# Performance work log

Measured on AMD Instinct MI355X. Metric: run time of the kernel, lower is better.

Reference implementation:

```python
import jax, jax.numpy as jnp
import numpy as np
from jax import lax

B, T, IN = 32, 512, 32
SNN, TS, HID, HOR = 128, 4, 128, 96
K = 3
THR = 1.0
EPS = 1e-5


def _spike(x):
    # heaviside: fires when (mem - threshold) > 0
    return (x > 0).astype(x.dtype)


def _lif_scan(xs, beta, thr):
    """snntorch Leaky (reset_mechanism='subtract'): mem_t = beta*mem_{t-1} + x_t - spk_{t-1}*thr; spk_t = H(mem_t - thr).
    xs: (S, B, C); beta: (C,). Returns spikes (S,B,C) and membrane (S,B,C)."""
    def step(carry, x):
        mem, rst = carry
        mem = beta * mem + x - rst * thr
        spk = _spike(mem - thr)
        return (mem, lax.stop_gradient(spk)), (spk, mem)
    z = jnp.zeros(xs.shape[1:], xs.dtype)
    _, (spks, mems) = lax.scan(step, (z, z), xs)
    return spks, mems


def setup_inputs() -> dict:
    key = jax.random.key(0)
    ks = jax.random.split(key, 10)
    def rn(k, shape, scale=0.05):
        return jax.random.normal(k, shape, dtype=jnp.float32) * scale
    return {
        "x": jax.random.normal(ks[0], (B, T, IN), dtype=jnp.float32),
        "conv_w": rn(ks[1], (SNN * TS, IN, K)),
        "conv_b": jnp.zeros((SNN * TS,), jnp.float32),
        "bn1_g": jnp.ones((SNN * TS,), jnp.float32),
        "bn1_b": jnp.zeros((SNN * TS,), jnp.float32),
        "beta1": jnp.full((SNN,), 0.9, jnp.float32),
        "bn2_g": jnp.ones((SNN,), jnp.float32),
        "bn2_b": jnp.zeros((SNN,), jnp.float32),
        "beta2": jnp.full((SNN,), 0.9, jnp.float32),
        "gru_wih": rn(ks[2], (3 * HID, IN + SNN)),
        "gru_whh": rn(ks[3], (3 * HID, HID)),
        "gru_bih": jnp.zeros((3 * HID,), jnp.float32),
        "gru_bhh": jnp.zeros((3 * HID,), jnp.float32),
        "q_w": rn(ks[4], (HID, HID)), "q_b": jnp.zeros((HID,), jnp.float32),
        "k_w": rn(ks[5], (HID, HID)), "k_b": jnp.zeros((HID,), jnp.float32),
        "v_w": rn(ks[6], (HID, HID)), "v_b": jnp.zeros((HID,), jnp.float32),
        "bn3_g": jnp.ones((HID,), jnp.float32),
        "bn3_b": jnp.zeros((HID,), jnp.float32),
        "head_w": rn(ks[7], (HOR, HID)),
        "head_b": jnp.zeros((HOR,), jnp.float32),
    }


def reference(x, conv_w, conv_b, bn1_g, bn1_b, beta1, bn2_g, bn2_b, beta2,
              gru_wih, gru_whh, gru_bih, gru_bhh, q_w, q_b, k_w, k_b, v_w, v_b,
              bn3_g, bn3_b, head_w, head_b):
    beta1 = jnp.clip(beta1, 0.0, 0.99)
    beta2 = jnp.clip(beta2, 0.0, 0.99)
    # --- ConvSpikeEncoder: Conv1d -> BatchNorm1d (training stats) -> LIF scan ---
    h = lax.conv_general_dilated(x.transpose(0, 2, 1), conv_w, (1,), [(K // 2, K // 2)],
                                 dimension_numbers=('NCH', 'OIH', 'NCH'))
    h = h + conv_b[None, :, None]  # (B, SNN*TS, T)
    m = h.mean((0, 2), keepdims=True)
    v = jnp.var(h, (0, 2), keepdims=True)
    h = (h - m) * lax.rsqrt(v + EPS) * bn1_g[None, :, None] + bn1_b[None, :, None]
    # (B, SNN*TS, T) -> (T*TS, B, SNN), step index = t*TS + s
    h = h.transpose(0, 2, 1).reshape(B, T * TS, SNN).transpose(1, 0, 2)
    spk_enc, _ = _lif_scan(h, beta1, THR)  # (T*TS, B, SNN)
    # --- per-step BatchNorm1d over batch dim, then second LIF ---
    m2 = spk_enc.mean(1, keepdims=True)
    v2 = jnp.var(spk_enc, 1, keepdims=True)
    h2 = (spk_enc - m2) * lax.rsqrt(v2 + EPS) * bn2_g + bn2_b
    _, mem_rec = _lif_scan(h2, beta2, THR)  # (T*TS, B, SNN)
    # --- downsample membrane: mean over TS sub-steps ---
    mem_down = mem_rec.transpose(1, 0, 2).reshape(B, T, TS, SNN).mean(2)  # (B, T, SNN)
    hc = jnp.concatenate([x, mem_down], -1)  # (B, T, IN+SNN)
    # --- GRU (PyTorch gate order r,z,n) ---
    def gstep(hprev, xt):
        gi = xt @ gru_wih.T + gru_bih
        gh = hprev @ gru_whh.T + gru_bhh
        ir, iz, inn = jnp.split(gi, 3, -1)
        hr, hz, hn = jnp.split(gh, 3, -1)
        r = jax.nn.sigmoid(ir + hr)
        zg = jax.nn.sigmoid(iz + hz)
        n = jnp.tanh(inn + r * hn)
        hnew = (1.0 - zg) * n + zg * hprev
        return hnew, hnew
    _, gru_seq = lax.scan(gstep, jnp.zeros((B, HID), x.dtype), hc.transpose(1, 0, 2))
    g = gru_seq.transpose(1, 0, 2)  # (B, T, HID)
    # --- SpikingAttention: sigmoid(QK^T*scale) @ V, mean over T, BatchNorm ---
    Q = g @ q_w.T + q_b
    Kk = g @ k_w.T + k_b
    V = g @ v_w.T + v_b
    attn = jax.nn.sigmoid(jnp.einsum('btc,bsc->bts', Q, Kk) * (HID ** -0.5))
    out = jnp.einsum('bts,bsc->btc', attn, V).mean(1)  # (B, HID)
    m3 = out.mean(0, keepdims=True)
    v3 = jnp.var(out, 0, keepdims=True)
    out = (out - m3) * lax.rsqrt(v3 + EPS) * bn3_g + bn3_b
    return out @ head_w.T + head_b  # (B, HOR)
```

## Files before the change

kernel.cpp:

```cpp
#include <hip/hip_runtime.h>
#include <math.h>

#define EPSV 1e-5f

#if __has_builtin(__builtin_amdgcn_exp2f)
#define EXP2F(x) __builtin_amdgcn_exp2f(x)
#else
#define EXP2F(x) exp2f(x)
#endif
#if __has_builtin(__builtin_amdgcn_rcpf)
#define RCPF(x) __builtin_amdgcn_rcpf(x)
#else
#define RCPF(x) (1.0f/(x))
#endif

__device__ __forceinline__ float fsigmoid(float x){
  return RCPF(1.0f + EXP2F(-1.4426950408889634f * x));
}
__device__ __forceinline__ float ftanh(float x){
  return RCPF(0.5f + 0.5f * EXP2F(-2.8853900817779268f * x)) - 1.0f;
}
__device__ __forceinline__ unsigned short f2bf(float f){
  unsigned u = __float_as_uint(f);
  return (unsigned short)((u + 0x7FFFu + ((u >> 16) & 1u)) >> 16);
}

typedef __attribute__((ext_vector_type(8))) short bf16x8;
typedef __attribute__((ext_vector_type(8))) short s16x8;
typedef __attribute__((ext_vector_type(4))) float f32x4;
typedef __attribute__((ext_vector_type(2))) _Float16 f16x2;
typedef __attribute__((ext_vector_type(8))) _Float16 f16x8;

#if __has_builtin(__builtin_amdgcn_fdot2)
#define FDOT2(a,b,c) __builtin_amdgcn_fdot2(a,b,c,false)
#else
__device__ __forceinline__ float FDOT2(f16x2 a, f16x2 b, float c){
  return c + (float)a[0]*(float)b[0] + (float)a[1]*(float)b[1];
}
#endif

__device__ __forceinline__ float dot8(f16x8 w, f16x8 h, float acc){
  f16x2 w0 = {w[0],w[1]}, w1 = {w[2],w[3]}, w2 = {w[4],w[5]}, w3 = {w[6],w[7]};
  f16x2 h0 = {h[0],h[1]}, h1 = {h[2],h[3]}, h2 = {h[4],h[5]}, h3 = {h[6],h[7]};
  acc = FDOT2(w0,h0,acc); acc = FDOT2(w1,h1,acc);
  acc = FDOT2(w2,h2,acc); acc = FDOT2(w3,h3,acc);
  return acc;
}

__global__ __launch_bounds__(256) void k_conv(const float* __restrict__ x, const float* __restrict__ w,
        const float* __restrict__ cb, float* __restrict__ hp, float* __restrict__ s1g,
        float* __restrict__ s2g, unsigned short* __restrict__ x_bf){
  __shared__ float xs[32*321];
  __shared__ float ws[32*97];
  __shared__ float bs[32];
  const int tid = threadIdx.x;
  const int t0 = blockIdx.x * 8;
  const int n0 = blockIdx.y * 8;
  for (int idx = tid; idx < 32*10*32; idx += 256){
    int bq = idx / 320; int rem = idx - bq*320; int tt = rem >> 5; int i = rem & 31;
    int tg = t0 - 1 + tt;
    float v = 0.f;
    if (tg >= 0 && tg < 512) v = x[(bq*512 + tg)*32 + i];
    xs[bq*321 + tt*32 + i] = v;
  }
  for (int idx = tid; idx < 32*96; idx += 256){
    int row = idx / 96; int within = idx - row*96;
    int ss = row >> 3; int nl = row & 7;
    int c = ss*128 + n0 + nl;
    ws[row*97 + within] = w[c*96 + within];
  }
  if (tid < 32){
    int ss = tid >> 3, nl = tid & 7;
    bs[tid] = cb[ss*128 + n0 + nl];
  }
  __syncthreads();
  if (blockIdx.y == 0){
    for (int idx = tid; idx < 32*8*32; idx += 256){
      int bq = idx >> 8; int rem = idx & 255; int tt = rem >> 5; int i = rem & 31;
      x_bf[(bq*512 + t0 + tt)*32 + i] = f2bf(xs[bq*321 + (tt+1)*32 + i]);
    }
  }
  const int b = tid & 31;
  const int nl = tid >> 5;
  float acc[4][8];
  #pragma unroll
  for (int ss = 0; ss < 4; ++ss){
    float bv = bs[ss*8 + nl];
    #pragma unroll
    for (int t = 0; t < 8; ++t) acc[ss][t] = bv;
  }
  for (int i = 0; i < 32; ++i){
    #pragma unroll
    for (int k = 0; k < 3; ++k){
      float w0 = ws[(0*8+nl)*97 + i*3 + k];
      float w1 = ws[(1*8+nl)*97 + i*3 + k];
      float w2 = ws[(2*8+nl)*97 + i*3 + k];
      float w3 = ws[(3*8+nl)*97 + i*3 + k];
      #pragma unroll
      for (int t = 0; t < 8; ++t){
        float xv = xs[b*321 + (t+k)*32 + i];
        acc[0][t] += xv*w0; acc[1][t] += xv*w1; acc[2][t] += xv*w2; acc[3][t] += xv*w3;
      }
    }
  }
  #pragma unroll
  for (int ss = 0; ss < 4; ++ss){
    int n = n0 + nl;
    float s1 = 0.f, s2 = 0.f;
    #pragma unroll
    for (int t = 0; t < 8; ++t){
      float v = acc[ss][t];
      int s = (t0 + t)*4 + ss;
      hp[s*4096 + n*32 + b] = v;
      s1 += v; s2 += v*v;
    }
    #pragma unroll
    for (int off = 1; off < 32; off <<= 1){
      s1 += __shfl_xor(s1, off);
      s2 += __shfl_xor(s2, off);
    }
    if (b == 0){
      int c = ss*128 + n;
      atomicAdd(&s1g[c], s1);
      atomicAdd(&s2g[c], s2);
    }
  }
}

__global__ __launch_bounds__(256) void k_cvt_all(const float* __restrict__ wih,
        const float* __restrict__ qw, const float* __restrict__ kw, const float* __restrict__ vw,
        const float* __restrict__ whh,
        unsigned short* __restrict__ wih_bf, unsigned short* __restrict__ wqkv_bf,
        _Float16* __restrict__ whh_h,
        const float* __restrict__ s1g, const float* __restrict__ s2g,
        const float* __restrict__ g, const float* __restrict__ bb,
        float* __restrict__ a1, float* __restrict__ b1){
  if (blockIdx.x >= 624){
    int c = (blockIdx.x - 624)*256 + threadIdx.x;
    if (c < 512){
      float m = s1g[c] * (1.f/16384.f);
      float v = s2g[c] * (1.f/16384.f) - m*m;
      float sc = g[c] * rsqrtf(v + EPSV);
      a1[c] = sc;
      b1[c] = bb[c] - m*sc;
    }
    return;
  }
  int i = blockIdx.x*256 + threadIdx.x;
  if (i < 61440){ wih_bf[i] = f2bf(wih[i]); return; }
  int r = i - 61440;
  if (r < 16384){ wqkv_bf[r] = f2bf(qw[r]); return; }
  r -= 16384;
  if (r < 16384){ wqkv_bf[16384 + r] = f2bf(kw[r]); return; }
  r -= 16384;
  if (r < 16384){ wqkv_bf[32768 + r] = f2bf(vw[r]); return; }
  r -= 16384;
  if (r < 49152){ whh_h[r] = (_Float16)whh[r]; }
}

__global__ __launch_bounds__(64) void k_lif(const float* __restrict__ hp,
        const float* __restrict__ a1, const float* __restrict__ b1,
        const float* __restrict__ beta1, const float* __restrict__ g2v, const float* __restrict__ b2v,
        const float* __restrict__ beta2, unsigned short* __restrict__ md_t){
  const int tid = threadIdx.x;
  const int b = tid & 31;
  const int n = blockIdx.x * 2 + (tid >> 5);
  float a1r0 = a1[0*128+n], a1r1 = a1[1*128+n], a1r2 = a1[2*128+n], a1r3 = a1[3*128+n];
  float b1r0 = b1[0*128+n], b1r1 = b1[1*128+n], b1r2 = b1[2*128+n], b1r3 = b1[3*128+n];
  float be1 = fminf(fmaxf(beta1[n], 0.f), 0.99f);
  float be2 = fminf(fmaxf(beta2[n], 0.f), 0.99f);
  float g2 = g2v[n], bb2 = b2v[n];
  float m1 = 0.f, r1 = 0.f, m2 = 0.f, r2 = 0.f;
  const float* base = hp + n*32 + b;
  float c0 = base[0], c1 = base[4096], c2 = base[2*4096], c3 = base[3*4096];
  const float* p1 = base + 16384;
  float d0 = p1[0], d1 = p1[4096], d2 = p1[2*4096], d3 = p1[3*4096];
  const float* p2 = base + 2*16384;
  float e0 = p2[0], e1 = p2[4096], e2 = p2[2*4096], e3 = p2[3*4096];

#define LIF_STEP(CV, A1R, B1R) { \
    float x1 = CV*A1R + B1R; \
    m1 = be1*m1 + x1 - r1; \
    bool sp = (m1 > 1.0f); \
    unsigned long long mk = __ballot(sp); \
    float spk = sp ? 1.f : 0.f; r1 = spk; \
    unsigned hf = (tid & 32) ? (unsigned)(mk >> 32) : (unsigned)mk; \
    float mean = (float)__popc(hf) * 0.03125f; \
    float var = mean - mean*mean; \
    float h2 = (spk - mean) * rsqrtf(var + EPSV) * g2 + bb2; \
    m2 = be2*m2 + h2 - r2; \
    r2 = (m2 > 1.0f) ? 1.f : 0.f; \
    accd += m2; }

  for (int t = 0; t < 512; ++t){
    float f0 = 0.f, f1 = 0.f, f2 = 0.f, f3 = 0.f;
    if (t < 509){
      const float* nb = base + (size_t)(t+3)*16384;
      f0 = nb[0]; f1 = nb[4096]; f2 = nb[2*4096]; f3 = nb[3*4096];
    }
    float accd = 0.f;
    LIF_STEP(c0, a1r0, b1r0)
    LIF_STEP(c1, a1r1, b1r1)
    LIF_STEP(c2, a1r2, b1r2)
    LIF_STEP(c3, a1r3, b1r3)
    md_t[((t*128) + n)*32 + b] = f2bf(accd * 0.25f);
    c0 = d0; c1 = d1; c2 = d2; c3 = d3;
    d0 = e0; d1 = e1; d2 = e2; d3 = e3;
    e0 = f0; e1 = f1; e2 = f2; e3 = f3;
  }
#undef LIF_STEP
}

__global__ __launch_bounds__(256) void k_mm_gi(const unsigned short* __restrict__ xbf,
        const unsigned short* __restrict__ md_t, const unsigned short* __restrict__ wihbf,
        const float* __restrict__ bih, float* __restrict__ gi2){
  const int tid = threadIdx.x;
  const int w = tid >> 6, l = tid & 63;
  const int c16 = l & 15, kg = l >> 4;
  const int m0 = (blockIdx.x*4 + w) * 16;
  const int mrow = m0 + c16;
  const int bb = mrow >> 9, tt = mrow & 511;
  bf16x8 a0 = *(const bf16x8*)&xbf[(size_t)mrow*32 + kg*8];
  const unsigned short* mt = md_t + (size_t)tt*4096 + bb;
  unsigned short tmp[4][8];
  #pragma unroll
  for (int f = 0; f < 4; ++f)
    #pragma unroll
    for (int e = 0; e < 8; ++e)
      tmp[f][e] = mt[(kg*8 + f*32 + e)*32];
  bf16x8 a1 = *(bf16x8*)tmp[0];
  bf16x8 a2 = *(bf16x8*)tmp[1];
  bf16x8 a3 = *(bf16x8*)tmp[2];
  bf16x8 a4 = *(bf16x8*)tmp[3];
  for (int nt2 = 0; nt2 < 8; ++nt2){
    int n0 = nt2*16;
    const unsigned short* wr = &wihbf[(size_t)(      n0 + c16)*160 + kg*8];
    const unsigned short* wz = &wihbf[(size_t)(128 + n0 + c16)*160 + kg*8];
    const unsigned short* wn = &wihbf[(size_t)(256 + n0 + c16)*160 + kg*8];
    f32x4 ar = {0.f,0.f,0.f,0.f}, az = {0.f,0.f,0.f,0.f}, an = {0.f,0.f,0.f,0.f};
    #pragma unroll
    for (int c = 0; c < 5; ++c){
      bf16x8 br = *(const bf16x8*)(wr + c*32);
      bf16x8 bz = *(const bf16x8*)(wz + c*32);
      bf16x8 bn = *(const bf16x8*)(wn + c*32);
      bf16x8 aa = (c == 0) ? a0 : (c == 1) ? a1 : (c == 2) ? a2 : (c == 3) ? a3 : a4;
      ar = __builtin_amdgcn_mfma_f32_16x16x32_bf16(aa, br, ar, 0, 0, 0);
      az = __builtin_amdgcn_mfma_f32_16x16x32_bf16(aa, bz, az, 0, 0, 0);
      an = __builtin_amdgcn_mfma_f32_16x16x32_bf16(aa, bn, an, 0, 0, 0);
    }
    float br_ = bih[n0 + c16], bz_ = bih[128 + n0 + c16], bn_ = bih[256 + n0 + c16];
    int jj = n0 + c16;
    #pragma unroll
    for (int r = 0; r < 4; ++r){
      float4 o = { ar[r] + br_, az[r] + bz_, an[r] + bn_, 0.f };
      *(float4*)&gi2[(size_t)(m0 + kg*4 + r)*512 + jj*4] = o;
    }
  }
}

template<int SEL>
__device__ __forceinline__ float dpp_qp(float x){
  return __int_as_float(__builtin_amdgcn_mov_dpp(__float_as_int(x), SEL, 0xF, 0xF, true));
}
__global__ __launch_bounds__(256, 1) void k_gru(const float* __restrict__ gi2, const _Float16* __restrict__ whh_h,
        const float* __restrict__ bhh, unsigned short* __restrict__ gout_bf){
  const int b = blockIdx.x;
  const int tid = threadIdx.x;
  const int j = tid >> 1;
  const int half = tid & 1;
  const int k0 = half * 64;
  __shared__ _Float16 hs[2][144];
  const _Float16* wbr = whh_h + (size_t)(      j)*128 + k0;
  const _Float16* wbz = whh_h + (size_t)(128 + j)*128 + k0;
  const _Float16* wbn = whh_h + (size_t)(256 + j)*128 + k0;
  f16x8 wr[8], wz[8], wn[8];
  #pragma unroll
  for (int i = 0; i < 8; ++i){
    wr[i] = *(const f16x8*)(wbr + i*8);
    wz[i] = *(const f16x8*)(wbz + i*8);
    wn[i] = *(const f16x8*)(wbn + i*8);
  }
  float bh_r = 0.f, bh_z = 0.f, bh_n = 0.f;
  if (!half){
    bh_r = bhh[j]; bh_z = bhh[128+j]; bh_n = bhh[256+j];
  }
  const float* gib = gi2 + (size_t)b*512*512 + j*4;
  f32x4 G[4], N[4];
  #pragma unroll
  for (int u = 0; u < 4; ++u){
    G[u] = *(const f32x4*)(gib + (size_t)u*512);
    N[u] = *(const f32x4*)(gib + (size_t)(4+u)*512);
  }
  if (tid < 128) hs[0][tid] = (_Float16)0.f;
  float hprev = 0.f;
  __syncthreads();
  for (int g = 0; g < 128; ++g){
    f32x4 N2[4];
    if (g < 126){
      #pragma unroll
      for (int u = 0; u < 4; ++u)
        N2[u] = *(const f32x4*)(gib + (size_t)(4*(g+2)+u)*512);
    } else {
      #pragma unroll
      for (int u = 0; u < 4; ++u) N2[u] = (f32x4){0.f,0.f,0.f,0.f};
    }
    #pragma unroll
    for (int u = 0; u < 4; ++u){
      const int t = g*4 + u;
      const f16x8* hq = (const f16x8*)&hs[t & 1][k0];
      f16x8 h0 = hq[0], h1 = hq[1], h2 = hq[2], h3 = hq[3],
            h4 = hq[4], h5 = hq[5], h6 = hq[6], h7 = hq[7];
      float ar0 = 0.f, ar1 = 0.f, az0 = 0.f, az1 = 0.f, an0 = 0.f, an1 = 0.f;
      ar0 = dot8(wr[0],h0,ar0); ar0 = dot8(wr[1],h1,ar0); ar0 = dot8(wr[2],h2,ar0); ar0 = dot8(wr[3],h3,ar0);
      ar1 = dot8(wr[4],h4,ar1); ar1 = dot8(wr[5],h5,ar1); ar1 = dot8(wr[6],h6,ar1); ar1 = dot8(wr[7],h7,ar1);
      az0 = dot8(wz[0],h0,az0); az0 = dot8(wz[1],h1,az0); az0 = dot8(wz[2],h2,az0); az0 = dot8(wz[3],h3,az0);
      az1 = dot8(wz[4],h4,az1); az1 = dot8(wz[5],h5,az1); az1 = dot8(wz[6],h6,az1); az1 = dot8(wz[7],h7,az1);
      an0 = dot8(wn[0],h0,an0); an0 = dot8(wn[1],h1,an0); an0 = dot8(wn[2],h2,an0); an0 = dot8(wn[3],h3,an0);
      an1 = dot8(wn[4],h4,an1); an1 = dot8(wn[5],h5,an1); an1 = dot8(wn[6],h6,an1); an1 = dot8(wn[7],h7,an1);
      float ar = ar0 + ar1, az = az0 + az1, an = an0 + an1;
      ar += dpp_qp<0xB1>(ar);
      az += dpp_qp<0xB1>(az);
      an += dpp_qp<0xB1>(an);
      if (!half){
        float r = fsigmoid(G[u][0] + ar + bh_r);
        float z = fsigmoid(G[u][1] + az + bh_z);
        float nn = ftanh(G[u][2] + r*(an + bh_n));
        float hn = (1.f - z)*nn + z*hprev;
        hprev = hn;
        hs[(t + 1) & 1][j] = (_Float16)hn;
        gout_bf[((size_t)b*512 + t)*128 + j] = f2bf(hn);
      }
      __syncthreads();
    }
    #pragma unroll
    for (int u = 0; u < 4; ++u){ G[u] = N[u]; N[u] = N2[u]; }
  }
}

__global__ __launch_bounds__(256) void k_mm_qkv(const unsigned short* __restrict__ gbf,
        const unsigned short* __restrict__ wbf, const float* __restrict__ qb2,
        const float* __restrict__ kb2, const float* __restrict__ vb2,
        unsigned short* __restrict__ Qbf, unsigned short* __restrict__ Kbf, float* __restrict__ Vb){
  const int tid = threadIdx.x;
  const int w = tid >> 6, l = tid & 63;
  const int c16 = l & 15, kg = l >> 4;
  const int m0 = (blockIdx.x*4 + w) * 16;
  const unsigned short* gp = &gbf[(size_t)(m0 + c16)*128 + kg*8];
  bf16x8 a0 = *(const bf16x8*)(gp + 0);
  bf16x8 a1 = *(const bf16x8*)(gp + 32);
  bf16x8 a2 = *(const bf16x8*)(gp + 64);
  bf16x8 a3 = *(const bf16x8*)(gp + 96);
  for (int nt = 0; nt < 24; ++nt){
    int n0 = nt*16;
    const unsigned short* wp = &wbf[(size_t)(n0 + c16)*128 + kg*8];
    bf16x8 b0 = *(const bf16x8*)(wp + 0);
    bf16x8 b1 = *(const bf16x8*)(wp + 32);
    bf16x8 b2 = *(const bf16x8*)(wp + 64);
    bf16x8 b3 = *(const bf16x8*)(wp + 96);
    f32x4 acc = {0.f,0.f,0.f,0.f};
    acc = __builtin_amdgcn_mfma_f32_16x16x32_bf16(a0, b0, acc, 0, 0, 0);
    acc = __builtin_amdgcn_mfma_f32_16x16x32_bf16(a1, b1, acc, 0, 0, 0);
    acc = __builtin_amdgcn_mfma_f32_16x16x32_bf16(a2, b2, acc, 0, 0, 0);
    acc = __builtin_amdgcn_mfma_f32_16x16x32_bf16(a3, b3, acc, 0, 0, 0);
    int n = n0 + c16;
    if (n < 128){
      float bias = qb2[n];
      #pragma unroll
      for (int r = 0; r < 4; ++r)
        Qbf[(size_t)(m0 + kg*4 + r)*128 + n] = f2bf(acc[r] + bias);
    } else if (n < 256){
      float bias = kb2[n-128];
      #pragma unroll
      for (int r = 0; r < 4; ++r)
        Kbf[(size_t)(m0 + kg*4 + r)*128 + (n-128)] = f2bf(acc[r] + bias);
    } else {
      float bias = vb2[n-256];
      #pragma unroll
      for (int r = 0; r < 4; ++r)
        Vb[(size_t)(m0 + kg*4 + r)*128 + (n-256)] = acc[r] + bias;
    }
  }
}

__global__ __launch_bounds__(256) void k_attn(const unsigned short* __restrict__ Qbf,
        const unsigned short* __restrict__ Kbf, const float* __restrict__ Vb,
        float* __restrict__ out0){
  __shared__ float avs[64];
  const int tid = threadIdx.x;
  const int b  = blockIdx.x;
  const int st = blockIdx.y;
  const int w  = tid >> 6;
  const int l  = tid & 63;
  const int c16 = l & 15;
  const int kg  = l >> 4;
  const float SC = 0.08838834764831845f;
  const unsigned short* kp = Kbf + ((size_t)(b*512 + st*64 + w*16 + c16))*128 + kg*8;
  bf16x8 a0 = *(const bf16x8*)(kp + 0);
  bf16x8 a1 = *(const bf16x8*)(kp + 32);
  bf16x8 a2 = *(const bf16x8*)(kp + 64);
  bf16x8 a3 = *(const bf16x8*)(kp + 96);
  const unsigned short* qb = Qbf + ((size_t)(b*512 + c16))*128 + kg*8;
  float ps0 = 0.f, ps1 = 0.f, ps2 = 0.f, ps3 = 0.f;
  for (int tt = 0; tt < 32; ++tt){
    const unsigned short* qp = qb + (size_t)tt*16*128;
    bf16x8 b0 = *(const bf16x8*)(qp + 0);
    bf16x8 b1 = *(const bf16x8*)(qp + 32);
    bf16x8 b2 = *(const bf16x8*)(qp + 64);
    bf16x8 b3 = *(const bf16x8*)(qp + 96);
    f32x4 acc = {0.f, 0.f, 0.f, 0.f};
    acc = __builtin_amdgcn_mfma_f32_16x16x32_bf16(a0, b0, acc, 0, 0, 0);
    acc = __builtin_amdgcn_mfma_f32_16x16x32_bf16(a1, b1, acc, 0, 0, 0);
    acc = __builtin_amdgcn_mfma_f32_16x16x32_bf16(a2, b2, acc, 0, 0, 0);
    acc = __builtin_amdgcn_mfma_f32_16x16x32_bf16(a3, b3, acc, 0, 0, 0);
    ps0 += fsigmoid(acc[0]*SC);
    ps1 += fsigmoid(acc[1]*SC);
    ps2 += fsigmoid(acc[2]*SC);
    ps3 += fsigmoid(acc[3]*SC);
  }
  #pragma unroll
  for (int off = 1; off < 16; off <<= 1){
    ps0 += __shfl_xor(ps0, off);
    ps1 += __shfl_xor(ps1, off);
    ps2 += __shfl_xor(ps2, off);
    ps3 += __shfl_xor(ps3, off);
  }
  if (c16 == 0){
    int sl = w*16 + kg*4;
    avs[sl + 0] = ps0 * (1.f/512.f);
    avs[sl + 1] = ps1 * (1.f/512.f);
    avs[sl + 2] = ps2 * (1.f/512.f);
    avs[sl + 3] = ps3 * (1.f/512.f);
  }
  __syncthreads();
  const int c = tid & 127;
  const int sh = tid >> 7;
  const float* vb = Vb + ((size_t)(b*512 + st*64 + sh*32))*128 + c;
  float acc = 0.f;
  #pragma unroll 8
  for (int sl = 0; sl < 32; ++sl)
    acc += avs[sh*32 + sl] * vb[(size_t)sl*128];
  atomicAdd(&out0[b*128 + c], acc);
}

__global__ __launch_bounds__(256) void k_final(const float* __restrict__ out0,
        const float* __restrict__ g3, const float* __restrict__ b3,
        const float* __restrict__ hw, const float* __restrict__ hb, float* __restrict__ out){
  __shared__ float on[2][132];
  const int tid = threadIdx.x;
  const int b0 = blockIdx.x * 2;
  if (tid < 128){
    int c = tid;
    float s = 0.f;
    #pragma unroll 8
    for (int bq = 0; bq < 32; ++bq) s += out0[bq*128 + c];
    float m = s * (1.f/32.f);
    float v = 0.f;
    #pragma unroll 8
    for (int bq = 0; bq < 32; ++bq){ float d = out0[bq*128 + c] - m; v += d*d; }
    v *= (1.f/32.f);
    float sc = g3[c] * rsqrtf(v + EPSV);
    float sh = b3[c] - m*sc;
    on[0][c] = out0[(b0+0)*128 + c]*sc + sh;
    on[1][c] = out0[(b0+1)*128 + c]*sc + sh;
  }
  __syncthreads();
  for (int o = tid; o < 2*96; o += 256){
    int bl = o / 96, hh = o - bl*96;
    float acc = hb[hh];
    for (int k = 0; k < 128; ++k) acc += on[bl][k] * hw[hh*128 + k];
    out[(b0 + bl)*96 + hh] = acc;
  }
}

extern "C" void kernel_launch(void* const* d_in, const int* in_sizes, int n_in,
                              void* d_out, int out_size, void* d_ws, size_t ws_size,
                              hipStream_t stream){
  const float* x      = (const float*)d_in[0];
  const float* conv_w = (const float*)d_in[1];
  const float* conv_b = (const float*)d_in[2];
  const float* bn1_g  = (const float*)d_in[3];
  const float* bn1_b  = (const float*)d_in[4];
  const float* beta1  = (const float*)d_in[5];
  const float* bn2_g  = (const float*)d_in[6];
  const float* bn2_b  = (const float*)d_in[7];
  const float* beta2  = (const float*)d_in[8];
  const float* g_wih  = (const float*)d_in[9];
  const float* g_whh  = (const float*)d_in[10];
  const float* g_bih  = (const float*)d_in[11];
  const float* g_bhh  = (const float*)d_in[12];
  const float* q_w    = (const float*)d_in[13];
  const float* q_b    = (const float*)d_in[14];
  const float* k_w    = (const float*)d_in[15];
  const float* k_b    = (const float*)d_in[16];
  const float* v_w    = (const float*)d_in[17];
  const float* v_b    = (const float*)d_in[18];
  const float* bn3_g  = (const float*)d_in[19];
  const float* bn3_b  = (const float*)d_in[20];
  const float* head_w = (const float*)d_in[21];
  const float* head_b = (const float*)d_in[22];

  char* ws = (char*)d_ws;
  float* hp            = (float*)ws;
  unsigned short* md_t = (unsigned short*)(ws + 37748736);
  unsigned short* g_bf = (unsigned short*)(ws + 37748736);
  unsigned short* x_bf = (unsigned short*)(ws + 41943040);
  unsigned short* wih_bf  = (unsigned short*)(ws + 42991616);
  unsigned short* wqkv_bf = (unsigned short*)(ws + 43114496);
  _Float16* whh_h      = (_Float16*)(ws + 43212800);
  float* s1g  = (float*)(ws + 50331648);
  float* s2g  = (float*)(ws + 50331648 + 2048);
  float* out0 = (float*)(ws + 50331648 + 4096);
  float* a1   = (float*)(ws + 50331648 + 20480);
  float* b1   = (float*)(ws + 50331648 + 22528);
  float* gi2 = (float*)ws;
  unsigned short* Qbf = (unsigned short*)ws;
  unsigned short* Kbf = (unsigned short*)(ws + 4194304);
  float* Vb  = (float*)(ws + 8388608);

  (void)hipMemsetAsync(ws + 50331648, 0, 20480, stream);

  k_conv<<<dim3(64, 16), 256, 0, stream>>>(x, conv_w, conv_b, hp, s1g, s2g, x_bf);
  k_cvt_all<<<626, 256, 0, stream>>>(g_wih, q_w, k_w, v_w, g_whh, wih_bf, wqkv_bf, whh_h,
                                     s1g, s2g, bn1_g, bn1_b, a1, b1);
  k_lif<<<64, 64, 0, stream>>>(hp, a1, b1, beta1, bn2_g, bn2_b, beta2, md_t);
  k_mm_gi<<<256, 256, 0, stream>>>(x_bf, md_t, wih_bf, g_bih, gi2);
  k_gru<<<32, 256, 0, stream>>>(gi2, whh_h, g_bhh, g_bf);
  k_mm_qkv<<<256, 256, 0, stream>>>(g_bf, wqkv_bf, q_b, k_b, v_b, Qbf, Kbf, Vb);
  k_attn<<<dim3(32, 8), 256, 0, stream>>>(Qbf, Kbf, Vb, out0);
  k_final<<<16, 256, 0, stream>>>(out0, bn3_g, bn3_b, head_w, head_b, (float*)d_out);
}
```

Before: 587.4 us.

## Fuse weight conversion into conv, fold BN1 stats into LIF, store GRU gates as bf16

The weight-conversion blocks are appended to the conv launch as extra blocks, which removes one kernel launch. The BN1 scale and shift are now computed inside the LIF kernel straight from the accumulated sums, so the separate a1/b1 buffers are gone. The GRU input-gate precompute is written as bf16 instead of fp32, which halves the traffic into the latency-bound recurrent kernel. The cost is reduced precision in the gate pre-activations, and the conversion blocks now depend on sharing a launch with the conv work.

```diff
diff --git a/kernel.cpp b/kernel.cpp
--- a/kernel.cpp
+++ b/kernel.cpp
@@ -24,9 +24,11 @@
   unsigned u = __float_as_uint(f);
   return (unsigned short)((u + 0x7FFFu + ((u >> 16) & 1u)) >> 16);
 }
+__device__ __forceinline__ float bf2f(unsigned short u){
+  return __uint_as_float(((unsigned)u) << 16);
+}
 
 typedef __attribute__((ext_vector_type(8))) short bf16x8;
-typedef __attribute__((ext_vector_type(8))) short s16x8;
 typedef __attribute__((ext_vector_type(4))) float f32x4;
 typedef __attribute__((ext_vector_type(2))) _Float16 f16x2;
 typedef __attribute__((ext_vector_type(8))) _Float16 f16x8;
@@ -47,15 +49,32 @@
   return acc;
 }
 
-__global__ __launch_bounds__(256) void k_conv(const float* __restrict__ x, const float* __restrict__ w,
+__global__ __launch_bounds__(256) void k_convcvt(const float* __restrict__ x, const float* __restrict__ w,
         const float* __restrict__ cb, float* __restrict__ hp, float* __restrict__ s1g,
-        float* __restrict__ s2g, unsigned short* __restrict__ x_bf){
+        float* __restrict__ s2g, unsigned short* __restrict__ x_bf,
+        const float* __restrict__ wih, const float* __restrict__ qw, const float* __restrict__ kw,
+        const float* __restrict__ vw, const float* __restrict__ whh,
+        unsigned short* __restrict__ wih_bf, unsigned short* __restrict__ wqkv_bf,
+        _Float16* __restrict__ whh_h){
+  const int tid = threadIdx.x;
+  if (blockIdx.x >= 1024){
+    int i = (blockIdx.x - 1024)*256 + tid;
+    if (i < 61440){ wih_bf[i] = f2bf(wih[i]); return; }
+    int r = i - 61440;
+    if (r < 16384){ wqkv_bf[r] = f2bf(qw[r]); return; }
+    r -= 16384;
+    if (r < 16384){ wqkv_bf[16384 + r] = f2bf(kw[r]); return; }
+    r -= 16384;
+    if (r < 16384){ wqkv_bf[32768 + r] = f2bf(vw[r]); return; }
+    r -= 16384;
+    if (r < 49152){ whh_h[r] = (_Float16)whh[r]; }
+    return;
+  }
   __shared__ float xs[32*321];
   __shared__ float ws[32*97];
   __shared__ float bs[32];
-  const int tid = threadIdx.x;
-  const int t0 = blockIdx.x * 8;
-  const int n0 = blockIdx.y * 8;
+  const int t0 = (blockIdx.x >> 4) * 8;
+  const int n0 = (blockIdx.x & 15) * 8;
   for (int idx = tid; idx < 32*10*32; idx += 256){
     int bq = idx / 320; int rem = idx - bq*320; int tt = rem >> 5; int i = rem & 31;
     int tg = t0 - 1 + tt;
@@ -74,7 +93,7 @@
     bs[tid] = cb[ss*128 + n0 + nl];
   }
   __syncthreads();
-  if (blockIdx.y == 0){
+  if ((blockIdx.x & 15) == 0){
     for (int idx = tid; idx < 32*8*32; idx += 256){
       int bq = idx >> 8; int rem = idx & 255; int tt = rem >> 5; int i = rem & 31;
       x_bf[(bq*512 + t0 + tt)*32 + i] = f2bf(xs[bq*321 + (tt+1)*32 + i]);
@@ -127,46 +146,24 @@
   }
 }
 
-__global__ __launch_bounds__(256) void k_cvt_all(const float* __restrict__ wih,
-        const float* __restrict__ qw, const float* __restrict__ kw, const float* __restrict__ vw,
-        const float* __restrict__ whh,
-        unsigned short* __restrict__ wih_bf, unsigned short* __restrict__ wqkv_bf,
-        _Float16* __restrict__ whh_h,
+__global__ __launch_bounds__(64) void k_lif(const float* __restrict__ hp,
         const float* __restrict__ s1g, const float* __restrict__ s2g,
-        const float* __restrict__ g, const float* __restrict__ bb,
-        float* __restrict__ a1, float* __restrict__ b1){
-  if (blockIdx.x >= 624){
-    int c = (blockIdx.x - 624)*256 + threadIdx.x;
-    if (c < 512){
-      float m = s1g[c] * (1.f/16384.f);
-      float v = s2g[c] * (1.f/16384.f) - m*m;
-      float sc = g[c] * rsqrtf(v + EPSV);
-      a1[c] = sc;
-      b1[c] = bb[c] - m*sc;
-    }
-    return;
-  }
-  int i = blockIdx.x*256 + threadIdx.x;
-  if (i < 61440){ wih_bf[i] = f2bf(wih[i]); return; }
-  int r = i - 61440;
-  if (r < 16384){ wqkv_bf[r] = f2bf(qw[r]); return; }
-  r -= 16384;
-  if (r < 16384){ wqkv_bf[16384 + r] = f2bf(kw[r]); return; }
-  r -= 16384;
-  if (r < 16384){ wqkv_bf[32768 + r] = f2bf(vw[r]); return; }
-  r -= 16384;
-  if (r < 49152){ whh_h[r] = (_Float16)whh[r]; }
-}
-
-__global__ __launch_bounds__(64) void k_lif(const float* __restrict__ hp,
-        const float* __restrict__ a1, const float* __restrict__ b1,
+        const float* __restrict__ g1v, const float* __restrict__ b1v,
         const float* __restrict__ beta1, const float* __restrict__ g2v, const float* __restrict__ b2v,
         const float* __restrict__ beta2, unsigned short* __restrict__ md_t){
   const int tid = threadIdx.x;
   const int b = tid & 31;
   const int n = blockIdx.x * 2 + (tid >> 5);
-  float a1r0 = a1[0*128+n], a1r1 = a1[1*128+n], a1r2 = a1[2*128+n], a1r3 = a1[3*128+n];
-  float b1r0 = b1[0*128+n], b1r1 = b1[1*128+n], b1r2 = b1[2*128+n], b1r3 = b1[3*128+n];
+  float a1r[4], b1r[4];
+  #pragma unroll
+  for (int ss = 0; ss < 4; ++ss){
+    int c = ss*128 + n;
+    float m = s1g[c] * (1.f/16384.f);
+    float v = s2g[c] * (1.f/16384.f) - m*m;
+    float sc = g1v[c] * rsqrtf(v + EPSV);
+    a1r[ss] = sc;
+    b1r[ss] = b1v[c] - m*sc;
+  }
   float be1 = fminf(fmaxf(beta1[n], 0.f), 0.99f);
   float be2 = fminf(fmaxf(beta2[n], 0.f), 0.99f);
   float g2 = g2v[n], bb2 = b2v[n];
@@ -199,10 +196,10 @@
       f0 = nb[0]; f1 = nb[4096]; f2 = nb[2*4096]; f3 = nb[3*4096];
     }
     float accd = 0.f;
-    LIF_STEP(c0, a1r0, b1r0)
-    LIF_STEP(c1, a1r1, b1r1)
-    LIF_STEP(c2, a1r2, b1r2)
-    LIF_STEP(c3, a1r3, b1r3)
+    LIF_STEP(c0, a1r[0], b1r[0])
+    LIF_STEP(c1, a1r[1], b1r[1])
+    LIF_STEP(c2, a1r[2], b1r[2])
+    LIF_STEP(c3, a1r[3], b1r[3])
     md_t[((t*128) + n)*32 + b] = f2bf(accd * 0.25f);
     c0 = d0; c1 = d1; c2 = d2; c3 = d3;
     d0 = e0; d1 = e1; d2 = e2; d3 = e3;
@@ -213,7 +210,7 @@
 
 __global__ __launch_bounds__(256) void k_mm_gi(const unsigned short* __restrict__ xbf,
         const unsigned short* __restrict__ md_t, const unsigned short* __restrict__ wihbf,
-        const float* __restrict__ bih, float* __restrict__ gi2){
+        const float* __restrict__ bih, unsigned short* __restrict__ gi2b){
   const int tid = threadIdx.x;
   const int w = tid >> 6, l = tid & 63;
   const int c16 = l & 15, kg = l >> 4;
@@ -252,8 +249,8 @@
     int jj = n0 + c16;
     #pragma unroll
     for (int r = 0; r < 4; ++r){
-      float4 o = { ar[r] + br_, az[r] + bz_, an[r] + bn_, 0.f };
-      *(float4*)&gi2[(size_t)(m0 + kg*4 + r)*512 + jj*4] = o;
+      ushort4 o = { f2bf(ar[r] + br_), f2bf(az[r] + bz_), f2bf(an[r] + bn_), 0 };
+      *(ushort4*)&gi2b[(size_t)(m0 + kg*4 + r)*512 + jj*4] = o;
     }
   }
 }
@@ -262,8 +259,9 @@
 __device__ __forceinline__ float dpp_qp(float x){
   return __int_as_float(__builtin_amdgcn_mov_dpp(__float_as_int(x), SEL, 0xF, 0xF, true));
 }
-__global__ __launch_bounds__(256, 1) void k_gru(const float* __restrict__ gi2, const _Float16* __restrict__ whh_h,
-        const float* __restrict__ bhh, unsigned short* __restrict__ gout_bf){
+__global__ __launch_bounds__(256, 1) void k_gru(const unsigned short* __restrict__ gi2b,
+        const _Float16* __restrict__ whh_h, const float* __restrict__ bhh,
+        unsigned short* __restrict__ gout_bf){
   const int b = blockIdx.x;
   const int tid = threadIdx.x;
   const int j = tid >> 1;
@@ -284,25 +282,25 @@
   if (!half){
     bh_r = bhh[j]; bh_z = bhh[128+j]; bh_n = bhh[256+j];
   }
-  const float* gib = gi2 + (size_t)b*512*512 + j*4;
-  f32x4 G[4], N[4];
+  const unsigned short* gib = gi2b + (size_t)b*512*512 + j*4;
+  ushort4 G[4], N[4];
   #pragma unroll
   for (int u = 0; u < 4; ++u){
-    G[u] = *(const f32x4*)(gib + (size_t)u*512);
-    N[u] = *(const f32x4*)(gib + (size_t)(4+u)*512);
+    G[u] = *(const ushort4*)(gib + (size_t)u*512);
+    N[u] = *(const ushort4*)(gib + (size_t)(4+u)*512);
   }
   if (tid < 128) hs[0][tid] = (_Float16)0.f;
   float hprev = 0.f;
   __syncthreads();
   for (int g = 0; g < 128; ++g){
-    f32x4 N2[4];
+    ushort4 N2[4];
     if (g < 126){
       #pragma unroll
       for (int u = 0; u < 4; ++u)
-        N2[u] = *(const f32x4*)(gib + (size_t)(4*(g+2)+u)*512);
+        N2[u] = *(const ushort4*)(gib + (size_t)(4*(g+2)+u)*512);
     } else {
       #pragma unroll
-      for (int u = 0; u < 4; ++u) N2[u] = (f32x4){0.f,0.f,0.f,0.f};
+      for (int u = 0; u < 4; ++u) N2[u] = (ushort4){0,0,0,0};
     }
     #pragma unroll
     for (int u = 0; u < 4; ++u){
@@ -322,9 +320,9 @@
       az += dpp_qp<0xB1>(az);
       an += dpp_qp<0xB1>(an);
       if (!half){
-        float r = fsigmoid(G[u][0] + ar + bh_r);
-        float z = fsigmoid(G[u][1] + az + bh_z);
-        float nn = ftanh(G[u][2] + r*(an + bh_n));
+        float r = fsigmoid(bf2f(G[u].x) + ar + bh_r);
+        float z = fsigmoid(bf2f(G[u].y) + az + bh_z);
+        float nn = ftanh(bf2f(G[u].z) + r*(an + bh_n));
         float hn = (1.f - z)*nn + z*hprev;
         hprev = hn;
         hs[(t + 1) & 1][j] = (_Float16)hn;
@@ -510,21 +508,18 @@
   float* s1g  = (float*)(ws + 50331648);
   float* s2g  = (float*)(ws + 50331648 + 2048);
   float* out0 = (float*)(ws + 50331648 + 4096);
-  float* a1   = (float*)(ws + 50331648 + 20480);
-  float* b1   = (float*)(ws + 50331648 + 22528);
-  float* gi2 = (float*)ws;
-  unsigned short* Qbf = (unsigned short*)ws;
-  unsigned short* Kbf = (unsigned short*)(ws + 4194304);
-  float* Vb  = (float*)(ws + 8388608);
+  unsigned short* gi2b = (unsigned short*)ws;
+  unsigned short* Qbf  = (unsigned short*)ws;
+  unsigned short* Kbf  = (unsigned short*)(ws + 4194304);
+  float* Vb   = (float*)(ws + 8388608);
 
   (void)hipMemsetAsync(ws + 50331648, 0, 20480, stream);
 
-  k_conv<<<dim3(64, 16), 256, 0, stream>>>(x, conv_w, conv_b, hp, s1g, s2g, x_bf);
-  k_cvt_all<<<626, 256, 0, stream>>>(g_wih, q_w, k_w, v_w, g_whh, wih_bf, wqkv_bf, whh_h,
-                                     s1g, s2g, bn1_g, bn1_b, a1, b1);
-  k_lif<<<64, 64, 0, stream>>>(hp, a1, b1, beta1, bn2_g, bn2_b, beta2, md_t);
-  k_mm_gi<<<256, 256, 0, stream>>>(x_bf, md_t, wih_bf, g_bih, gi2);
-  k_gru<<<32, 256, 0, stream>>>(gi2, whh_h, g_bhh, g_bf);
+  k_convcvt<<<1648, 256, 0, stream>>>(x, conv_w, conv_b, hp, s1g, s2g, x_bf,
+                                      g_wih, q_w, k_w, v_w, g_whh, wih_bf, wqkv_bf, whh_h);
+  k_lif<<<64, 64, 0, stream>>>(hp, s1g, s2g, bn1_g, bn1_b, beta1, bn2_g, bn2_b, beta2, md_t);
+  k_mm_gi<<<256, 256, 0, stream>>>(x_bf, md_t, wih_bf, g_bih, gi2b);
+  k_gru<<<32, 256, 0, stream>>>(gi2b, whh_h, g_bhh, g_bf);
   k_mm_qkv<<<256, 256, 0, stream>>>(g_bf, wqkv_bf, q_b, k_b, v_b, Qbf, Kbf, Vb);
   k_attn<<<dim3(32, 8), 256, 0, stream>>>(Qbf, Kbf, Vb, out0);
   k_final<<<16, 256, 0, stream>>>(out0, bn3_g, bn3_b, head_w, head_b, (float*)d_out);
```

Result: faster. 547.1 us (median of 2 runs) (-6.8%).
